# Optimization experiments

Measured on AMD Instinct MI355X. Metric: run time of the kernel, lower is better.

The kernel has to match this reference:

```python
import jax, jax.numpy as jnp
import numpy as np

B, S, H, I, E, K = 2, 512, 768, 3072, 8, 1
LB_COEF = 0.01


def _xavier(key, shape, fan_in, fan_out):
    limit = np.sqrt(6.0 / (fan_in + fan_out)).astype(np.float32)
    return jax.random.uniform(key, shape, jnp.float32, -limit, limit)


def setup_inputs() -> dict:
    key = jax.random.key(0)
    k0, k1, k2, k3 = jax.random.split(key, 4)
    return {
        "hidden_states": jax.random.normal(k0, (B, S, H), jnp.float32),
        "gate_w": _xavier(k1, (E, H), H, E),          # nn.Linear(H, E).weight
        "gate_b": jnp.zeros((E,), jnp.float32),
        "w1": _xavier(k2, (E, I, H), H, I),           # per-expert Linear(H, I).weight
        "b1": jnp.zeros((E, I), jnp.float32),
        "w2": _xavier(k3, (E, H, I), I, H),           # per-expert Linear(I, H).weight
        "b2": jnp.zeros((E, H), jnp.float32),
    }


def reference(hidden_states, gate_w, gate_b, w1, b1, w2, b2):
    b, s, h = hidden_states.shape
    x = hidden_states.reshape(-1, h)                      # [T, H]
    gate_logits = x @ gate_w.T + gate_b                   # [T, E]
    top_vals, top_idx = jax.lax.top_k(gate_logits, K)     # [T, K]
    # softmax over the (single) selected logit in fp32 -> all ones, kept for fidelity
    gate_weights = jax.nn.softmax(top_vals.astype(jnp.float32), axis=-1)  # [T, K]

    # load balancing loss (torch.var is unbiased, ddof=1)
    gate_mean = gate_logits.mean(axis=0)                  # [E]
    gate_var = gate_logits.var(axis=0, ddof=1)            # [E]
    lb_loss = LB_COEF * (gate_var / (gate_mean ** 2 + 1e-8)).mean()

    # dense per-expert FFN (exact math; combine picks the routed expert)
    hmid = jnp.einsum('th,eih->tei', x, w1) + b1          # [T, E, I]
    hmid = jax.nn.gelu(hmid, approximate=False)           # torch nn.GELU (erf)
    y = jnp.einsum('tei,ehi->teh', hmid, w2) + b2         # [T, E, H]

    sel = top_idx[:, 0]                                   # [T]
    y_sel = jnp.take_along_axis(y, sel[:, None, None], axis=1)[:, 0]  # [T, H]
    out = y_sel * gate_weights[:, 0:1]                    # weight == 1.0 for k=1
    return out.reshape(b, s, h), lb_loss
```

## Files before the change

kernel.cpp:

```cpp
#include <hip/hip_runtime.h>
#include <hip/hip_bf16.h>
#include <math.h>

#define Hdim 768
#define Idim 3072
#define Tn   1024
#define En   8
#define CAP  256
#define LD2  136

using v4f     = __attribute__((ext_vector_type(4))) float;
using short8  = __attribute__((ext_vector_type(8))) short;
using short4v = __attribute__((ext_vector_type(4))) short;

__device__ inline unsigned short f2bf(float f) {
    unsigned u = __float_as_uint(f);
    u += 0x7fffu + ((u >> 16) & 1u);
    return (unsigned short)(u >> 16);
}
__device__ inline short4v pack4(float4 v) {
    return short4v{ (short)f2bf(v.x), (short)f2bf(v.y), (short)f2bf(v.z), (short)f2bf(v.w) };
}
__device__ __forceinline__ void gl2lds16(const unsigned short* g, unsigned short* l) {
    __builtin_amdgcn_global_load_lds(
        (const __attribute__((address_space(1))) void*)g,
        (__attribute__((address_space(3))) void*)l, 16, 0, 0);
}

__global__ __launch_bounds__(256) void gatecat_kernel(
    const float* __restrict__ x, const float* __restrict__ gw, const float* __restrict__ gb,
    const float* __restrict__ b2,
    float* __restrict__ psum, float* __restrict__ psumsq,
    int* __restrict__ gcur, int* __restrict__ perm,
    unsigned short* __restrict__ xb, float* __restrict__ out)
{
    __shared__ float gws[8 * 772];
    __shared__ float lg[8][8];
    __shared__ int ssel[8];
    __shared__ int sslot[8];
    int tid = threadIdx.x;
    long t0 = (long)blockIdx.x * 8;
    for (int i = tid; i < 8 * 768; i += 256) gws[(i / 768) * 772 + (i % 768)] = gw[i];
    __syncthreads();

    int tok = tid >> 5, e = (tid >> 2) & 7, qr = tid & 3;
    const float4* xp = (const float4*)(x + (t0 + tok) * Hdim) + qr * 48;
    const float4* gp = (const float4*)(gws + e * 772) + qr * 48;
    float a0 = 0.f, a1 = 0.f;
#pragma unroll 8
    for (int i = 0; i < 48; i += 2) {
        float4 xa = xp[i], ga = gp[i], xc = xp[i + 1], gc = gp[i + 1];
        a0 += xa.x * ga.x + xa.y * ga.y + xa.z * ga.z + xa.w * ga.w;
        a1 += xc.x * gc.x + xc.y * gc.y + xc.z * gc.z + xc.w * gc.w;
    }
    float acc = a0 + a1;
    acc += __shfl_xor(acc, 1);
    acc += __shfl_xor(acc, 2);
    if (qr == 0) lg[tok][e] = acc + gb[e];
    __syncthreads();

    if (tid < 8) {
        float best = lg[tid][0]; int bi = 0;
        for (int j = 1; j < 8; j++) { float v = lg[tid][j]; if (v > best) { best = v; bi = j; } }
        ssel[tid] = bi;
        sslot[tid] = atomicAdd(&gcur[bi], 1);
    } else if (tid < 16) {
        int e2 = tid - 8;
        float s = 0.f, ss = 0.f;
        for (int t2 = 0; t2 < 8; t2++) { float v = lg[t2][e2]; s += v; ss += v * v; }
        psum[blockIdx.x * 8 + e2]   = s;
        psumsq[blockIdx.x * 8 + e2] = ss;
    }
    __syncthreads();

    int lane = tid & 63, wave = tid >> 6;
#pragma unroll
    for (int k = 0; k < 2; k++) {
        int tl = wave * 2 + k;
        long t = t0 + tl;
        int e2 = ssel[tl];
        int pos = sslot[tl];
        if (pos < CAP) {
            int slot = (e2 << 8) + pos;
            if (lane == 0) perm[slot] = (int)t;
            const float4* src  = (const float4*)(x + t * Hdim);
            const float4* bsrc = (const float4*)(b2 + (long)e2 * Hdim);
            unsigned short* dst = xb + (long)slot * Hdim;
            float4* odst = (float4*)(out + t * Hdim);
#pragma unroll
            for (int i = 0; i < 3; i++) {
                int c = lane + 64 * i;
                *(short4v*)(dst + c * 4) = pack4(src[c]);
                odst[c] = bsrc[c];
            }
        }
    }
}

__device__ __forceinline__ void gemm_tile_64x64(
    const unsigned short* __restrict__ Arow0, long lda,
    const float* __restrict__ Bn0, long ldb,
    int nloc, int m0, unsigned short* As, unsigned short* Bs, v4f acc[4])
{
    int tid = threadIdx.x;
    int lane = tid & 63, wave = tid >> 6;
    int quad = lane >> 4, l16 = lane & 15;

    const unsigned short* aG[4];
    unsigned short* aL[4];
#pragma unroll
    for (int i = 0; i < 4; i++) {
        int p = (wave * 4 + i) * 64 + lane;
        int row = p >> 4;
        int kc = (p & 15) ^ (row & 15);
        int m = m0 + row; int mm = m < nloc ? m : nloc - 1;
        aG[i] = Arow0 + (long)mm * lda + kc * 8;
        aL[i] = As + p * 8;
    }
    int kq5 = tid & 31, rb8 = tid >> 5;
    const float* bp = Bn0 + (long)rb8 * ldb + kq5 * 4;
    unsigned short* bw = Bs + rb8 * LD2 + kq5 * 4;

    float4 nb[8];
#pragma unroll
    for (int s = 0; s < 8; s++) nb[s] = *(const float4*)(bp + (long)(8 * s) * ldb);

    for (int kb = 0; kb < 768; kb += 128) {
        __syncthreads();
#pragma unroll
        for (int i = 0; i < 4; i++) gl2lds16(aG[i] + kb, aL[i]);
#pragma unroll
        for (int s = 0; s < 8; s++)
            *(short4v*)(bw + s * 8 * LD2) = pack4(nb[s]);
        __syncthreads();
        if (kb + 128 < 768) {
#pragma unroll
            for (int s = 0; s < 8; s++)
                nb[s] = *(const float4*)(bp + (long)(8 * s) * ldb + kb + 128);
        }
#pragma unroll
        for (int s = 0; s < 4; s++) {
            int r = (wave << 4) + l16;
            short8 af = *(const short8*)(As + r * 128 + (((s * 4 + quad) ^ (r & 15)) * 8));
#pragma unroll
            for (int j = 0; j < 4; j++) {
                short8 bf = *(const short8*)(Bs + (j * 16 + l16) * LD2 + s * 32 + quad * 8);
                acc[j] = __builtin_amdgcn_mfma_f32_16x16x32_bf16(af, bf, acc[j], 0, 0, 0);
            }
        }
    }
}

__global__ __launch_bounds__(256) void gemm1_kernel(
    const unsigned short* __restrict__ xb, const float* __restrict__ w1, const float* __restrict__ b1,
    const int* __restrict__ count,
    const float* __restrict__ psum, const float* __restrict__ psumsq,
    unsigned short* __restrict__ hmid, float* __restrict__ out_lb)
{
    int tid = threadIdx.x;
    if (blockIdx.x == 0 && blockIdx.y == 0 && blockIdx.z == 0 && tid < 64) {
        int e = tid & 7, c0 = (tid >> 3) * 16;
        float s = 0.f, ss = 0.f;
        for (int b = c0; b < c0 + 16; b++) { s += psum[b * 8 + e]; ss += psumsq[b * 8 + e]; }
        s  += __shfl_xor(s, 8);  s  += __shfl_xor(s, 16);  s  += __shfl_xor(s, 32);
        ss += __shfl_xor(ss, 8); ss += __shfl_xor(ss, 16); ss += __shfl_xor(ss, 32);
        if (tid < 8) {
            float mean = s * (1.0f / 1024.0f);
            float var  = (ss - s * mean) * (1.0f / 1023.0f);
            float r = var / (mean * mean + 1e-8f);
            r += __shfl_xor(r, 1); r += __shfl_xor(r, 2); r += __shfl_xor(r, 4);
            if (tid == 0) out_lb[0] = 0.01f * r * 0.125f;
        }
    }

    int e = blockIdx.z;
    int nloc = count[e]; if (nloc > CAP) nloc = CAP;
    int m0 = blockIdx.y << 6;
    if (m0 >= nloc) return;
    int n0 = blockIdx.x << 6;
    int off = e << 8;

    __shared__ __align__(16) unsigned short As[64 * 128];
    __shared__ __align__(16) unsigned short Bs[64 * LD2];

    int lane = tid & 63, wave = tid >> 6;
    int quad = lane >> 4, l16 = lane & 15;

    v4f acc[4];
#pragma unroll
    for (int j = 0; j < 4; j++) acc[j] = (v4f){0.f, 0.f, 0.f, 0.f};
    gemm_tile_64x64(xb + (long)off * Hdim, Hdim,
                    w1 + ((long)e * Idim + n0) * Hdim, Hdim,
                    nloc, m0, As, Bs, acc);

    int mr = (wave << 4) + quad * 4;
#pragma unroll
    for (int r = 0; r < 4; r++) {
        int m = m0 + mr + r;
        if (m >= nloc) continue;
        long slot = off + m;
#pragma unroll
        for (int j = 0; j < 4; j++) {
            int n = n0 + j * 16 + l16;
            float v = acc[j][r] + b1[e * Idim + n];
            float g = 0.5f * v * (1.0f + erff(v * 0.70710678118654752f));
            hmid[slot * Idim + n] = f2bf(g);
        }
    }
}

__global__ __launch_bounds__(256) void gemm2_kernel(
    const unsigned short* __restrict__ hmid, const float* __restrict__ w2,
    const int* __restrict__ count, const int* __restrict__ perm,
    float* __restrict__ out)
{
    int e = blockIdx.z;
    int nloc = count[e]; if (nloc > CAP) nloc = CAP;
    int m0 = blockIdx.y << 6;
    if (m0 >= nloc) return;
    int bx = blockIdx.x;
    int n0 = (bx % 12) << 6;
    int kc4 = bx / 12;
    long kbase = (long)kc4 * 768;
    int off = e << 8;

    __shared__ __align__(16) unsigned short As[64 * 128];
    __shared__ __align__(16) unsigned short Bs[64 * LD2];

    int tid = threadIdx.x;
    int lane = tid & 63, wave = tid >> 6;
    int quad = lane >> 4, l16 = lane & 15;

    v4f acc[4];
#pragma unroll
    for (int j = 0; j < 4; j++) acc[j] = (v4f){0.f, 0.f, 0.f, 0.f};
    gemm_tile_64x64(hmid + (long)off * Idim + kbase, Idim,
                    w2 + ((long)e * Hdim + n0) * Idim + kbase, Idim,
                    nloc, m0, As, Bs, acc);

    int mr = (wave << 4) + quad * 4;
#pragma unroll
    for (int r = 0; r < 4; r++) {
        int m = m0 + mr + r;
        if (m >= nloc) continue;
        int t = perm[off + m];
#pragma unroll
        for (int j = 0; j < 4; j++) {
            int n = n0 + j * 16 + l16;
            atomicAdd(out + (long)t * Hdim + n, acc[j][r]);
        }
    }
}

extern "C" void kernel_launch(void* const* d_in, const int* in_sizes, int n_in,
                              void* d_out, int out_size, void* d_ws, size_t ws_size,
                              hipStream_t stream)
{
    const float* x  = (const float*)d_in[0];
    const float* gw = (const float*)d_in[1];
    const float* gb = (const float*)d_in[2];
    const float* w1 = (const float*)d_in[3];
    const float* b1 = (const float*)d_in[4];
    const float* w2 = (const float*)d_in[5];
    const float* b2 = (const float*)d_in[6];
    float* out = (float*)d_out;

    int*   gcur   = (int*)d_ws;
    float* psum   = (float*)((char*)d_ws + 4352);
    float* psumsq = (float*)((char*)d_ws + 8448);
    int*   perm   = (int*)((char*)d_ws + 12544);
    unsigned short* xb   = (unsigned short*)((char*)d_ws + 32768);
    unsigned short* hmid = (unsigned short*)((char*)d_ws + (1u << 22));

    hipMemsetAsync(d_ws, 0, 32, stream);
    gatecat_kernel<<<128, 256, 0, stream>>>(x, gw, gb, b2, psum, psumsq, gcur, perm, xb, out);
    gemm1_kernel<<<dim3(48, 4, 8), 256, 0, stream>>>(xb, w1, b1, gcur, psum, psumsq, hmid,
                                                     out + (long)Tn * Hdim);
    gemm2_kernel<<<dim3(48, 4, 8), 256, 0, stream>>>(hmid, w2, gcur, perm, out);
}
```

Measured before the change: 226.9 us.

## Double-buffer LDS tiles and prefetch weights two stages ahead in MoE GEMMs

Replaces the single-buffered 64x64 GEMM tile loop with a ping-pong LDS scheme. The next A tile is loaded into the alternate buffer via global_load_lds while the current one feeds MFMAs, and fp32 weight rows are prefetched in registers two K-steps ahead. Explicit waitcnt plus one barrier per step replaces the two syncthreads per step. The goal is to hide global memory latency behind compute, at the cost of doubled LDS use and more registers, which may lower occupancy.

After: 237.7 us. 4.8% more time.

```diff
diff --git a/kernel.cpp b/kernel.cpp
--- a/kernel.cpp
+++ b/kernel.cpp
@@ -97,17 +97,20 @@
     }
 }
 
-__device__ __forceinline__ void gemm_tile_64x64(
+__device__ __forceinline__ void gemm_tile_64x64_pipe(
     const unsigned short* __restrict__ Arow0, long lda,
     const float* __restrict__ Bn0, long ldb,
-    int nloc, int m0, unsigned short* As, unsigned short* Bs, v4f acc[4])
+    int nloc, int m0,
+    unsigned short* As0, unsigned short* As1,
+    unsigned short* Bs0, unsigned short* Bs1,
+    v4f acc[4])
 {
     int tid = threadIdx.x;
     int lane = tid & 63, wave = tid >> 6;
     int quad = lane >> 4, l16 = lane & 15;
 
     const unsigned short* aG[4];
-    unsigned short* aL[4];
+    int aOff[4];
 #pragma unroll
     for (int i = 0; i < 4; i++) {
         int p = (wave * 4 + i) * 64 + lane;
@@ -115,38 +118,63 @@
         int kc = (p & 15) ^ (row & 15);
         int m = m0 + row; int mm = m < nloc ? m : nloc - 1;
         aG[i] = Arow0 + (long)mm * lda + kc * 8;
-        aL[i] = As + p * 8;
+        aOff[i] = p * 8;
     }
     int kq5 = tid & 31, rb8 = tid >> 5;
     const float* bp = Bn0 + (long)rb8 * ldb + kq5 * 4;
-    unsigned short* bw = Bs + rb8 * LD2 + kq5 * 4;
-
-    float4 nb[8];
-#pragma unroll
-    for (int s = 0; s < 8; s++) nb[s] = *(const float4*)(bp + (long)(8 * s) * ldb);
-
-    for (int kb = 0; kb < 768; kb += 128) {
-        __syncthreads();
-#pragma unroll
-        for (int i = 0; i < 4; i++) gl2lds16(aG[i] + kb, aL[i]);
-#pragma unroll
-        for (int s = 0; s < 8; s++)
-            *(short4v*)(bw + s * 8 * LD2) = pack4(nb[s]);
-        __syncthreads();
-        if (kb + 128 < 768) {
+    int bwOff = rb8 * LD2 + kq5 * 4;
+
+    float4 nb[2][8];
+
+#pragma unroll
+    for (int i = 0; i < 4; i++) gl2lds16(aG[i], As0 + aOff[i]);
+#pragma unroll
+    for (int s = 0; s < 8; s++) nb[0][s] = *(const float4*)(bp + (long)(8 * s) * ldb);
+#pragma unroll
+    for (int s = 0; s < 8; s++) nb[1][s] = *(const float4*)(bp + (long)(8 * s) * ldb + 128);
+#pragma unroll
+    for (int s = 0; s < 8; s++) *(short4v*)(Bs0 + bwOff + s * 8 * LD2) = pack4(nb[0][s]);
+#pragma unroll
+    for (int s = 0; s < 8; s++) nb[0][s] = *(const float4*)(bp + (long)(8 * s) * ldb + 256);
+    asm volatile("s_waitcnt lgkmcnt(0)" ::: "memory");
+    __builtin_amdgcn_s_barrier();
+    __builtin_amdgcn_sched_barrier(0);
+
+#pragma unroll
+    for (int t = 0; t < 6; t++) {
+        const int par = t & 1;
+        unsigned short* Asw = par ? As0 : As1;
+        unsigned short* Bsw = par ? Bs0 : Bs1;
+        const unsigned short* Asr = par ? As1 : As0;
+        const unsigned short* Bsr = par ? Bs1 : Bs0;
+
+        if (t + 1 < 6) {
+#pragma unroll
+            for (int i = 0; i < 4; i++) gl2lds16(aG[i] + (t + 1) * 128, Asw + aOff[i]);
 #pragma unroll
             for (int s = 0; s < 8; s++)
-                nb[s] = *(const float4*)(bp + (long)(8 * s) * ldb + kb + 128);
+                *(short4v*)(Bsw + bwOff + s * 8 * LD2) = pack4(nb[par ^ 1][s]);
+        }
+        if (t + 3 < 6) {
+#pragma unroll
+            for (int s = 0; s < 8; s++)
+                nb[par ^ 1][s] = *(const float4*)(bp + (long)(8 * s) * ldb + (t + 3) * 128);
         }
 #pragma unroll
         for (int s = 0; s < 4; s++) {
             int r = (wave << 4) + l16;
-            short8 af = *(const short8*)(As + r * 128 + (((s * 4 + quad) ^ (r & 15)) * 8));
+            short8 af = *(const short8*)(Asr + r * 128 + (((s * 4 + quad) ^ (r & 15)) * 8));
 #pragma unroll
             for (int j = 0; j < 4; j++) {
-                short8 bf = *(const short8*)(Bs + (j * 16 + l16) * LD2 + s * 32 + quad * 8);
+                short8 bf = *(const short8*)(Bsr + (j * 16 + l16) * LD2 + s * 32 + quad * 8);
                 acc[j] = __builtin_amdgcn_mfma_f32_16x16x32_bf16(af, bf, acc[j], 0, 0, 0);
             }
+        }
+        if (t + 1 < 6) {
+            if (t + 3 < 6) asm volatile("s_waitcnt vmcnt(8) lgkmcnt(0)" ::: "memory");
+            else           asm volatile("s_waitcnt vmcnt(0) lgkmcnt(0)" ::: "memory");
+            __builtin_amdgcn_s_barrier();
+            __builtin_amdgcn_sched_barrier(0);
         }
     }
 }
@@ -180,8 +208,8 @@
     int n0 = blockIdx.x << 6;
     int off = e << 8;
 
-    __shared__ __align__(16) unsigned short As[64 * 128];
-    __shared__ __align__(16) unsigned short Bs[64 * LD2];
+    __shared__ __align__(16) unsigned short As0[64 * 128], As1[64 * 128];
+    __shared__ __align__(16) unsigned short Bs0[64 * LD2], Bs1[64 * LD2];
 
     int lane = tid & 63, wave = tid >> 6;
     int quad = lane >> 4, l16 = lane & 15;
@@ -189,9 +217,9 @@
     v4f acc[4];
 #pragma unroll
     for (int j = 0; j < 4; j++) acc[j] = (v4f){0.f, 0.f, 0.f, 0.f};
-    gemm_tile_64x64(xb + (long)off * Hdim, Hdim,
-                    w1 + ((long)e * Idim + n0) * Hdim, Hdim,
-                    nloc, m0, As, Bs, acc);
+    gemm_tile_64x64_pipe(xb + (long)off * Hdim, Hdim,
+                         w1 + ((long)e * Idim + n0) * Hdim, Hdim,
+                         nloc, m0, As0, As1, Bs0, Bs1, acc);
 
     int mr = (wave << 4) + quad * 4;
 #pragma unroll
@@ -224,8 +252,8 @@
     long kbase = (long)kc4 * 768;
     int off = e << 8;
 
-    __shared__ __align__(16) unsigned short As[64 * 128];
-    __shared__ __align__(16) unsigned short Bs[64 * LD2];
+    __shared__ __align__(16) unsigned short As0[64 * 128], As1[64 * 128];
+    __shared__ __align__(16) unsigned short Bs0[64 * LD2], Bs1[64 * LD2];
 
     int tid = threadIdx.x;
     int lane = tid & 63, wave = tid >> 6;
@@ -234,9 +262,9 @@
     v4f acc[4];
 #pragma unroll
     for (int j = 0; j < 4; j++) acc[j] = (v4f){0.f, 0.f, 0.f, 0.f};
-    gemm_tile_64x64(hmid + (long)off * Idim + kbase, Idim,
-                    w2 + ((long)e * Hdim + n0) * Idim + kbase, Idim,
-                    nloc, m0, As, Bs, acc);
+    gemm_tile_64x64_pipe(hmid + (long)off * Idim + kbase, Idim,
+                         w2 + ((long)e * Hdim + n0) * Idim + kbase, Idim,
+                         nloc, m0, As0, As1, Bs0, Bs1, acc);
 
     int mr = (wave << 4) + quad * 4;
 #pragma unroll
```
